# Optimization experiments

Measured on AMD Instinct MI355X. Metric: run time of the kernel, lower is better.

The kernel has to match this reference:

```python
import jax, jax.numpy as jnp
import numpy as np

N, E, F_IN, H, C = 10000, 640000, 128, 128, 40


def setup_inputs() -> dict:
    key = jax.random.key(0)
    ks = jax.random.split(key, 8)
    x = jax.random.normal(ks[0], (N, F_IN), dtype=jnp.float32)
    edge_index = jax.random.randint(ks[1], (2, E), 0, N, dtype=jnp.int64)
    W1 = jax.random.normal(ks[2], (F_IN, H), dtype=jnp.float32) / np.sqrt(F_IN)
    b1 = jnp.zeros((H,), dtype=jnp.float32)
    W2 = jax.random.normal(ks[3], (H, H), dtype=jnp.float32) / np.sqrt(H)
    b2 = jnp.zeros((H,), dtype=jnp.float32)
    Wc = jax.random.normal(ks[4], (H, C), dtype=jnp.float32) / np.sqrt(H)
    bc = jnp.zeros((C,), dtype=jnp.float32)
    return {"x": x, "edge_index": edge_index, "W1": W1, "b1": b1,
            "W2": W2, "b2": b2, "Wc": Wc, "bc": bc}


def _gcn_conv(x, src, dst, norm, W, b):
    # GCNConv: out = D^{-1/2}(A+I)D^{-1/2} (x @ W) + b
    h = x @ W                               # [N, H]
    msg = h[src] * norm[:, None]            # gather + per-edge normalize
    out = jax.ops.segment_sum(msg, dst, num_segments=N)  # scatter-add
    return out + b


def reference(x, edge_index, W1, b1, W2, b2, Wc, bc):
    # add self-loops (as PyG GCNConv does by default)
    loops = jnp.arange(N, dtype=edge_index.dtype)
    src = jnp.concatenate([edge_index[0], loops])   # [E+N]
    dst = jnp.concatenate([edge_index[1], loops])   # [E+N]
    # symmetric normalization deg^{-1/2} with self-loops included
    deg = jax.ops.segment_sum(jnp.ones_like(dst, dtype=x.dtype), dst, num_segments=N)
    dinv = jax.lax.rsqrt(deg)                       # deg >= 1 due to self-loops
    norm = dinv[src] * dinv[dst]                    # [E+N]

    h = _gcn_conv(x, src, dst, norm, W1, b1)
    h = jax.nn.relu(h)
    h = _gcn_conv(h, src, dst, norm, W2, b2)
    logits = h @ Wc + bc                            # [N, C]
    return jax.nn.log_softmax(logits, axis=1)
```

## Files before the change

### kernel.cpp

```cpp
#include <hip/hip_runtime.h>
#include <hip/hip_fp16.h>
#include <math.h>

#define FDIM 128
#define CDIM 40
#define DMAX 192
#define NMAX 10240
#define SLICE_SHIFT 14
#define SLICE_SZ (1 << SLICE_SHIFT)

__device__ __forceinline__ uint2 pack_half4(float4 v) {
    __half2 p0 = __float22half2_rn(make_float2(v.x, v.y));
    __half2 p1 = __float22half2_rn(make_float2(v.z, v.w));
    uint2 u;
    u.x = *(unsigned int*)&p0;
    u.y = *(unsigned int*)&p1;
    return u;
}

__device__ __forceinline__ void unpack_add4(float acc[8], uint4 r) {
    __half2* p = (__half2*)&r;
    #pragma unroll
    for (int q = 0; q < 4; ++q) {
        float2 f = __half22float2(p[q]);
        acc[2 * q]     += f.x;
        acc[2 * q + 1] += f.y;
    }
}

__global__ __launch_bounds__(256) void k_hist(
        const int* __restrict__ dst, unsigned short* __restrict__ lrank,
        int* __restrict__ cnt, int e, int n) {
    __shared__ int h[NMAX];
    int tid = threadIdx.x;
    for (int i = tid; i < n; i += 256) h[i] = 0;
    __syncthreads();
    int base = (int)blockIdx.x << SLICE_SHIFT;
    int end = base + SLICE_SZ; if (end > e) end = e;
    for (int i = base + tid * 4; i < end; i += 1024) {
        if (i + 3 < end) {
            int4 d = *(const int4*)(dst + i);
            int p0 = atomicAdd(&h[d.x], 1);
            int p1 = atomicAdd(&h[d.y], 1);
            int p2 = atomicAdd(&h[d.z], 1);
            int p3 = atomicAdd(&h[d.w], 1);
            ushort4 r;
            r.x = (unsigned short)p0; r.y = (unsigned short)p1;
            r.z = (unsigned short)p2; r.w = (unsigned short)p3;
            *(ushort4*)(lrank + i) = r;
        } else {
            for (int k = i; k < end; ++k)
                lrank[k] = (unsigned short)atomicAdd(&h[dst[k]], 1);
        }
    }
    __syncthreads();
    int* c = cnt + (size_t)blockIdx.x * n;
    for (int i = tid; i < n; i += 256) c[i] = h[i];
}

__global__ __launch_bounds__(256) void k_scan(
        int* __restrict__ cnt, int* __restrict__ deg, int nslice, int n) {
    int v = blockIdx.x * 256 + threadIdx.x;
    if (v >= n) return;
    int s = 0;
    for (int b = 0; b < nslice; ++b) {
        int t = cnt[(size_t)b * n + v];
        cnt[(size_t)b * n + v] = s;
        s += t;
    }
    deg[v] = s;
}

__global__ __launch_bounds__(256) void k_mega(
        const float* __restrict__ A, const float* __restrict__ W,
        const int* __restrict__ deg, uint2* __restrict__ h16, int n,
        const int* __restrict__ src, const int* __restrict__ dst,
        const unsigned short* __restrict__ lrank, const int* __restrict__ base,
        unsigned short* __restrict__ col, int e, int gemm_blocks) {
    __shared__ float As[32][FDIM];
    int tid = threadIdx.x;
    if ((int)blockIdx.x < gemm_blocks) {
        int r0 = blockIdx.x * 32;
        for (int t = tid; t < 32 * 32; t += 256) {
            int r = t >> 5, c4 = t & 31;
            int gr = r0 + r;
            float4 v = make_float4(0.f, 0.f, 0.f, 0.f);
            if (gr < n) v = ((const float4*)A)[(size_t)gr * 32 + c4];
            ((float4*)As[r])[c4] = v;
        }
        __syncthreads();
        int cb = (tid & 31) * 4;
        int rb = (tid >> 5) * 4;
        float4 acc0 = make_float4(0,0,0,0), acc1 = acc0, acc2 = acc0, acc3 = acc0;
        for (int k = 0; k < FDIM; ++k) {
            float4 w = *(const float4*)(W + k * FDIM + cb);
            float a0 = As[rb + 0][k], a1 = As[rb + 1][k];
            float a2 = As[rb + 2][k], a3 = As[rb + 3][k];
            acc0.x += a0 * w.x; acc0.y += a0 * w.y; acc0.z += a0 * w.z; acc0.w += a0 * w.w;
            acc1.x += a1 * w.x; acc1.y += a1 * w.y; acc1.z += a1 * w.z; acc1.w += a1 * w.w;
            acc2.x += a2 * w.x; acc2.y += a2 * w.y; acc2.z += a2 * w.z; acc2.w += a2 * w.w;
            acc3.x += a3 * w.x; acc3.y += a3 * w.y; acc3.z += a3 * w.z; acc3.w += a3 * w.w;
        }
        float4 accs[4] = {acc0, acc1, acc2, acc3};
        #pragma unroll
        for (int i = 0; i < 4; ++i) {
            int gr = r0 + rb + i;
            if (gr < n) {
                float dinv = rsqrtf((float)(deg[gr] + 1));
                float4 v = accs[i];
                v.x *= dinv; v.y *= dinv; v.z *= dinv; v.w *= dinv;
                h16[(size_t)gr * 32 + (cb >> 2)] = pack_half4(v);
            }
        }
    } else {
        int g = ((int)blockIdx.x - gemm_blocks) * 256 + tid;
        int i4 = g * 4;
        if (i4 + 3 < e) {
            const int* bs = base + (size_t)(i4 >> SLICE_SHIFT) * n;
            int4 d = ((const int4*)dst)[g];
            int4 s = ((const int4*)src)[g];
            ushort4 lr = ((const ushort4*)lrank)[g];
            int p0 = bs[d.x] + lr.x;
            int p1 = bs[d.y] + lr.y;
            int p2 = bs[d.z] + lr.z;
            int p3 = bs[d.w] + lr.w;
            if (p0 < DMAX) col[(size_t)d.x * DMAX + p0] = (unsigned short)s.x;
            if (p1 < DMAX) col[(size_t)d.y * DMAX + p1] = (unsigned short)s.y;
            if (p2 < DMAX) col[(size_t)d.z * DMAX + p2] = (unsigned short)s.z;
            if (p3 < DMAX) col[(size_t)d.w * DMAX + p3] = (unsigned short)s.w;
        } else if (i4 < e) {
            for (int k = i4; k < e; ++k) {
                int d = dst[k];
                int p = base[(size_t)(k >> SLICE_SHIFT) * n + d] + lrank[k];
                if (p < DMAX) col[(size_t)d * DMAX + p] = (unsigned short)src[k];
            }
        }
    }
}

template <bool RELU>
__device__ __forceinline__ void agg_gather(
        float out8[8], const uint4* __restrict__ hs,
        const unsigned short* __restrict__ col, const int* __restrict__ deg,
        const float* __restrict__ bias, int node, int l) {
    int dn = deg[node];
    float dinv = rsqrtf((float)(dn + 1));
    if (dn > DMAX) dn = DMAX;
    const uint4* cl8 = (const uint4*)(col + (size_t)node * DMAX);
    float a0[8], a1[8];
    #pragma unroll
    for (int q = 0; q < 8; ++q) { a0[q] = 0.f; a1[q] = 0.f; }
    unpack_add4(a0, hs[(size_t)node * 16 + l]);
    int j = 0;
    for (; j + 8 <= dn; j += 8) {
        uint4 c = cl8[j >> 3];
        int s0 = c.x & 0xFFFF, s1 = c.x >> 16;
        int s2 = c.y & 0xFFFF, s3 = c.y >> 16;
        int s4 = c.z & 0xFFFF, s5 = c.z >> 16;
        int s6 = c.w & 0xFFFF, s7 = c.w >> 16;
        uint4 q0 = hs[(size_t)s0 * 16 + l];
        uint4 q1 = hs[(size_t)s1 * 16 + l];
        uint4 q2 = hs[(size_t)s2 * 16 + l];
        uint4 q3 = hs[(size_t)s3 * 16 + l];
        uint4 q4 = hs[(size_t)s4 * 16 + l];
        uint4 q5 = hs[(size_t)s5 * 16 + l];
        uint4 q6 = hs[(size_t)s6 * 16 + l];
        uint4 q7 = hs[(size_t)s7 * 16 + l];
        unpack_add4(a0, q0); unpack_add4(a1, q1);
        unpack_add4(a0, q2); unpack_add4(a1, q3);
        unpack_add4(a0, q4); unpack_add4(a1, q5);
        unpack_add4(a0, q6); unpack_add4(a1, q7);
    }
    const unsigned short* cl = col + (size_t)node * DMAX;
    for (; j < dn; ++j) unpack_add4(a0, hs[(size_t)cl[j] * 16 + l]);
    float4 b0 = ((const float4*)bias)[2 * l];
    float4 b1 = ((const float4*)bias)[2 * l + 1];
    float bb[8] = {b0.x, b0.y, b0.z, b0.w, b1.x, b1.y, b1.z, b1.w};
    #pragma unroll
    for (int q = 0; q < 8; ++q) {
        float v = dinv * (a0[q] + a1[q]) + bb[q];
        out8[q] = RELU ? fmaxf(v, 0.f) : v;
    }
}

__global__ __launch_bounds__(128) void k_agg_gemm(
        const uint4* __restrict__ hs1, const unsigned short* __restrict__ col,
        const int* __restrict__ deg, const float* __restrict__ b1,
        const float* __restrict__ W2, uint2* __restrict__ hs2, int n) {
    __shared__ float As[8][FDIM + 4];
    __shared__ float dl[8];
    int tid = threadIdx.x;
    int grp = tid >> 4, l = tid & 15;
    int node = blockIdx.x * 8 + grp;
    if (node < n) {
        float r8[8];
        agg_gather<true>(r8, hs1, col, deg, b1, node, l);
        float4* dst4 = (float4*)&As[grp][8 * l];
        dst4[0] = make_float4(r8[0], r8[1], r8[2], r8[3]);
        dst4[1] = make_float4(r8[4], r8[5], r8[6], r8[7]);
        if (l == 0) dl[grp] = rsqrtf((float)(deg[node] + 1));
    }
    __syncthreads();
    int cb = (tid & 31) * 4;
    int rb = (tid >> 5) * 2;
    float4 acc0 = make_float4(0,0,0,0), acc1 = acc0;
    for (int k = 0; k < FDIM; ++k) {
        float4 w = *(const float4*)(W2 + k * FDIM + cb);
        float x0 = As[rb][k], x1 = As[rb + 1][k];
        acc0.x += x0 * w.x; acc0.y += x0 * w.y; acc0.z += x0 * w.z; acc0.w += x0 * w.w;
        acc1.x += x1 * w.x; acc1.y += x1 * w.y; acc1.z += x1 * w.z; acc1.w += x1 * w.w;
    }
    int g0 = blockIdx.x * 8 + rb;
    if (g0 < n) {
        float s = dl[rb];
        float4 v = acc0;
        v.x *= s; v.y *= s; v.z *= s; v.w *= s;
        hs2[(size_t)g0 * 32 + (cb >> 2)] = pack_half4(v);
    }
    if (g0 + 1 < n) {
        float s = dl[rb + 1];
        float4 v = acc1;
        v.x *= s; v.y *= s; v.z *= s; v.w *= s;
        hs2[(size_t)(g0 + 1) * 32 + (cb >> 2)] = pack_half4(v);
    }
}

__global__ __launch_bounds__(128) void k_agg_cls(
        const uint4* __restrict__ hs2, const unsigned short* __restrict__ col,
        const int* __restrict__ deg, const float* __restrict__ b2,
        const float* __restrict__ Wc, const float* __restrict__ bc,
        float* __restrict__ out, int n) {
    __shared__ float As[8][FDIM + 4];
    int tid = threadIdx.x;
    int grp = tid >> 4, l = tid & 15;
    int node = blockIdx.x * 8 + grp;
    if (node < n) {
        float r8[8];
        agg_gather<false>(r8, hs2, col, deg, b2, node, l);
        float4* dst4 = (float4*)&As[grp][8 * l];
        dst4[0] = make_float4(r8[0], r8[1], r8[2], r8[3]);
        dst4[1] = make_float4(r8[4], r8[5], r8[6], r8[7]);
    }
    __syncthreads();
    int wv = tid >> 6, lane = tid & 63;
    #pragma unroll
    for (int ii = 0; ii < 4; ++ii) {
        int li = wv * 4 + ii;
        int nd = blockIdx.x * 8 + li;
        if (nd >= n) continue;
        const float* row = As[li];
        int c = (lane < CDIM) ? lane : (lane - 24);
        float acc = bc[c];
        for (int k = 0; k < FDIM; k += 4) {
            float a0 = row[k + 0], a1 = row[k + 1];
            float a2 = row[k + 2], a3 = row[k + 3];
            acc += a0 * Wc[(k + 0) * CDIM + c];
            acc += a1 * Wc[(k + 1) * CDIM + c];
            acc += a2 * Wc[(k + 2) * CDIM + c];
            acc += a3 * Wc[(k + 3) * CDIM + c];
        }
        float lv = (lane < CDIM) ? acc : -INFINITY;
        float m = lv;
        for (int off = 32; off > 0; off >>= 1) m = fmaxf(m, __shfl_down(m, off));
        m = __shfl(m, 0);
        float e = (lane < CDIM) ? expf(lv - m) : 0.0f;
        float s = e;
        for (int off = 32; off > 0; off >>= 1) s += __shfl_down(s, off);
        s = __shfl(s, 0);
        if (lane < CDIM) out[(size_t)nd * CDIM + lane] = lv - m - logf(s);
    }
}


extern "C" void kernel_launch(void* const* d_in, const int* in_sizes, int n_in,
                              void* d_out, int out_size, void* d_ws, size_t ws_size,
                              hipStream_t stream) {
    const float* x  = (const float*)d_in[0];
    const int*   ei = (const int*)d_in[1];
    const float* W1 = (const float*)d_in[2];
    const float* b1 = (const float*)d_in[3];
    const float* W2 = (const float*)d_in[4];
    const float* b2 = (const float*)d_in[5];
    const float* Wc = (const float*)d_in[6];
    const float* bc = (const float*)d_in[7];
    float* out = (float*)d_out;

    const int N = in_sizes[0] / FDIM;
    const int E = in_sizes[1] / 2;
    const int* srcp = ei;
    const int* dstp = ei + E;
    const int NSLICE = (E + SLICE_SZ - 1) >> SLICE_SHIFT;

    char* ws = (char*)d_ws;
    auto alloc = [&](size_t bytes) {
        char* p = ws;
        ws += (bytes + 255) & ~(size_t)255;
        return p;
    };
    int*            deg   = (int*)           alloc((size_t)N * 4);
    int*            cnt   = (int*)           alloc((size_t)NSLICE * N * 4);
    unsigned short* lrank = (unsigned short*)alloc((size_t)E * 2);
    unsigned short* col   = (unsigned short*)alloc((size_t)N * DMAX * 2);
    uint4*          h1h   = (uint4*)         alloc((size_t)N * 256);
    uint4*          h2h   = (uint4*)         alloc((size_t)N * 256);

    k_hist<<<NSLICE, 256, 0, stream>>>(dstp, lrank, cnt, E, N);

    k_scan<<<(N + 255) / 256, 256, 0, stream>>>(cnt, deg, NSLICE, N);

    int gb = (N + 31) / 32;
    int fb = (E / 4 + 255) / 256;
    k_mega<<<gb + fb, 256, 0, stream>>>(
        x, W1, deg, (uint2*)h1h, N, srcp, dstp, lrank, cnt, col, E, gb);

    k_agg_gemm<<<(N + 7) / 8, 128, 0, stream>>>(
        h1h, col, deg, b1, W2, (uint2*)h2h, N);

    k_agg_cls<<<(N + 7) / 8, 128, 0, stream>>>(
        h2h, col, deg, b2, Wc, bc, out, N);
}
```

Measured before the change: 160.2 us.

## Split each node's neighbor gather across two thread groups in aggregation kernels

The aggregation kernels now use 256 threads per block with two 16-lane groups per node. Each group gathers alternate 8-neighbor chunks, and the two partial sums are combined in shared memory before the bias, ReLU and normalization are applied. The aim is to double the memory-level parallelism of the latency-bound random gathers, since average degree is about 64. The cost is an extra shared-memory pass and barrier, twice the shared memory per block, and a GEMM phase where each thread now produces one row instead of two.

```diff
diff --git a/kernel.cpp b/kernel.cpp
--- a/kernel.cpp
+++ b/kernel.cpp
@@ -138,114 +138,132 @@
     }
 }
 
-template <bool RELU>
-__device__ __forceinline__ void agg_gather(
-        float out8[8], const uint4* __restrict__ hs,
-        const unsigned short* __restrict__ col, const int* __restrict__ deg,
-        const float* __restrict__ bias, int node, int l) {
-    int dn = deg[node];
-    float dinv = rsqrtf((float)(dn + 1));
-    if (dn > DMAX) dn = DMAX;
-    const uint4* cl8 = (const uint4*)(col + (size_t)node * DMAX);
+__device__ __forceinline__ void agg_gather_half(
+        float a[8], const uint4* __restrict__ hs,
+        const unsigned short* __restrict__ col, int node, int l, int dn,
+        int half) {
     float a0[8], a1[8];
     #pragma unroll
     for (int q = 0; q < 8; ++q) { a0[q] = 0.f; a1[q] = 0.f; }
-    unpack_add4(a0, hs[(size_t)node * 16 + l]);
-    int j = 0;
-    for (; j + 8 <= dn; j += 8) {
-        uint4 c = cl8[j >> 3];
-        int s0 = c.x & 0xFFFF, s1 = c.x >> 16;
-        int s2 = c.y & 0xFFFF, s3 = c.y >> 16;
-        int s4 = c.z & 0xFFFF, s5 = c.z >> 16;
-        int s6 = c.w & 0xFFFF, s7 = c.w >> 16;
-        uint4 q0 = hs[(size_t)s0 * 16 + l];
-        uint4 q1 = hs[(size_t)s1 * 16 + l];
-        uint4 q2 = hs[(size_t)s2 * 16 + l];
-        uint4 q3 = hs[(size_t)s3 * 16 + l];
-        uint4 q4 = hs[(size_t)s4 * 16 + l];
-        uint4 q5 = hs[(size_t)s5 * 16 + l];
-        uint4 q6 = hs[(size_t)s6 * 16 + l];
-        uint4 q7 = hs[(size_t)s7 * 16 + l];
-        unpack_add4(a0, q0); unpack_add4(a1, q1);
-        unpack_add4(a0, q2); unpack_add4(a1, q3);
-        unpack_add4(a0, q4); unpack_add4(a1, q5);
-        unpack_add4(a0, q6); unpack_add4(a1, q7);
-    }
-    const unsigned short* cl = col + (size_t)node * DMAX;
-    for (; j < dn; ++j) unpack_add4(a0, hs[(size_t)cl[j] * 16 + l]);
-    float4 b0 = ((const float4*)bias)[2 * l];
-    float4 b1 = ((const float4*)bias)[2 * l + 1];
-    float bb[8] = {b0.x, b0.y, b0.z, b0.w, b1.x, b1.y, b1.z, b1.w};
+    if (half == 0) unpack_add4(a0, hs[(size_t)node * 16 + l]);
+    if (dn > DMAX) dn = DMAX;
+    const uint4* cl8 = (const uint4*)(col + (size_t)node * DMAX);
+    int nchunk = (dn + 7) >> 3;
+    for (int c = half; c < nchunk; c += 2) {
+        uint4 cc = cl8[c];
+        int cnt = dn - (c << 3);
+        if (cnt >= 8) {
+            int s0 = cc.x & 0xFFFF, s1 = cc.x >> 16;
+            int s2 = cc.y & 0xFFFF, s3 = cc.y >> 16;
+            int s4 = cc.z & 0xFFFF, s5 = cc.z >> 16;
+            int s6 = cc.w & 0xFFFF, s7 = cc.w >> 16;
+            uint4 q0 = hs[(size_t)s0 * 16 + l];
+            uint4 q1 = hs[(size_t)s1 * 16 + l];
+            uint4 q2 = hs[(size_t)s2 * 16 + l];
+            uint4 q3 = hs[(size_t)s3 * 16 + l];
+            uint4 q4 = hs[(size_t)s4 * 16 + l];
+            uint4 q5 = hs[(size_t)s5 * 16 + l];
+            uint4 q6 = hs[(size_t)s6 * 16 + l];
+            uint4 q7 = hs[(size_t)s7 * 16 + l];
+            unpack_add4(a0, q0); unpack_add4(a1, q1);
+            unpack_add4(a0, q2); unpack_add4(a1, q3);
+            unpack_add4(a0, q4); unpack_add4(a1, q5);
+            unpack_add4(a0, q6); unpack_add4(a1, q7);
+        } else {
+            union { uint4 v; unsigned short u[8]; } uu;
+            uu.v = cc;
+            for (int t = 0; t < cnt; ++t)
+                unpack_add4(a0, hs[(size_t)uu.u[t] * 16 + l]);
+        }
+    }
     #pragma unroll
-    for (int q = 0; q < 8; ++q) {
-        float v = dinv * (a0[q] + a1[q]) + bb[q];
-        out8[q] = RELU ? fmaxf(v, 0.f) : v;
-    }
-}
-
-__global__ __launch_bounds__(128) void k_agg_gemm(
+    for (int q = 0; q < 8; ++q) a[q] = a0[q] + a1[q];
+}
+
+__global__ __launch_bounds__(256) void k_agg_gemm(
         const uint4* __restrict__ hs1, const unsigned short* __restrict__ col,
         const int* __restrict__ deg, const float* __restrict__ b1,
         const float* __restrict__ W2, uint2* __restrict__ hs2, int n) {
-    __shared__ float As[8][FDIM + 4];
-    __shared__ float dl[8];
+    __shared__ float As[16][FDIM + 4];
     int tid = threadIdx.x;
-    int grp = tid >> 4, l = tid & 15;
-    int node = blockIdx.x * 8 + grp;
+    int slot = tid >> 4, l = tid & 15;
+    int node = blockIdx.x * 8 + (slot & 7);
+    int half = slot >> 3;
     if (node < n) {
-        float r8[8];
-        agg_gather<true>(r8, hs1, col, deg, b1, node, l);
-        float4* dst4 = (float4*)&As[grp][8 * l];
-        dst4[0] = make_float4(r8[0], r8[1], r8[2], r8[3]);
-        dst4[1] = make_float4(r8[4], r8[5], r8[6], r8[7]);
-        if (l == 0) dl[grp] = rsqrtf((float)(deg[node] + 1));
-    }
-    __syncthreads();
-    int cb = (tid & 31) * 4;
-    int rb = (tid >> 5) * 2;
-    float4 acc0 = make_float4(0,0,0,0), acc1 = acc0;
+        float a[8];
+        agg_gather_half(a, hs1, col, node, l, deg[node], half);
+        float4* d4 = (float4*)&As[slot][8 * l];
+        d4[0] = make_float4(a[0], a[1], a[2], a[3]);
+        d4[1] = make_float4(a[4], a[5], a[6], a[7]);
+    }
+    __syncthreads();
+    int r = tid >> 5;
+    int k0 = (tid & 31) * 4;
+    int g = blockIdx.x * 8 + r;
+    if (g < n) {
+        float di = rsqrtf((float)(deg[g] + 1));
+        float4 p0 = *(float4*)&As[r][k0];
+        float4 p1 = *(float4*)&As[r + 8][k0];
+        float4 b = *(const float4*)(b1 + k0);
+        float4 v;
+        v.x = fmaxf(di * (p0.x + p1.x) + b.x, 0.f);
+        v.y = fmaxf(di * (p0.y + p1.y) + b.y, 0.f);
+        v.z = fmaxf(di * (p0.z + p1.z) + b.z, 0.f);
+        v.w = fmaxf(di * (p0.w + p1.w) + b.w, 0.f);
+        *(float4*)&As[r][k0] = v;
+    }
+    __syncthreads();
+    float4 acc = make_float4(0, 0, 0, 0);
     for (int k = 0; k < FDIM; ++k) {
-        float4 w = *(const float4*)(W2 + k * FDIM + cb);
-        float x0 = As[rb][k], x1 = As[rb + 1][k];
-        acc0.x += x0 * w.x; acc0.y += x0 * w.y; acc0.z += x0 * w.z; acc0.w += x0 * w.w;
-        acc1.x += x1 * w.x; acc1.y += x1 * w.y; acc1.z += x1 * w.z; acc1.w += x1 * w.w;
-    }
-    int g0 = blockIdx.x * 8 + rb;
-    if (g0 < n) {
-        float s = dl[rb];
-        float4 v = acc0;
-        v.x *= s; v.y *= s; v.z *= s; v.w *= s;
-        hs2[(size_t)g0 * 32 + (cb >> 2)] = pack_half4(v);
-    }
-    if (g0 + 1 < n) {
-        float s = dl[rb + 1];
-        float4 v = acc1;
-        v.x *= s; v.y *= s; v.z *= s; v.w *= s;
-        hs2[(size_t)(g0 + 1) * 32 + (cb >> 2)] = pack_half4(v);
-    }
-}
-
-__global__ __launch_bounds__(128) void k_agg_cls(
+        float4 w = *(const float4*)(W2 + k * FDIM + k0);
+        float a = As[r][k];
+        acc.x += a * w.x; acc.y += a * w.y; acc.z += a * w.z; acc.w += a * w.w;
+    }
+    if (g < n) {
+        float di = rsqrtf((float)(deg[g] + 1));
+        acc.x *= di; acc.y *= di; acc.z *= di; acc.w *= di;
+        hs2[(size_t)g * 32 + (k0 >> 2)] = pack_half4(acc);
+    }
+}
+
+__global__ __launch_bounds__(256) void k_agg_cls(
         const uint4* __restrict__ hs2, const unsigned short* __restrict__ col,
         const int* __restrict__ deg, const float* __restrict__ b2,
         const float* __restrict__ Wc, const float* __restrict__ bc,
         float* __restrict__ out, int n) {
-    __shared__ float As[8][FDIM + 4];
+    __shared__ float As[16][FDIM + 4];
     int tid = threadIdx.x;
-    int grp = tid >> 4, l = tid & 15;
-    int node = blockIdx.x * 8 + grp;
+    int slot = tid >> 4, l = tid & 15;
+    int node = blockIdx.x * 8 + (slot & 7);
+    int half = slot >> 3;
     if (node < n) {
-        float r8[8];
-        agg_gather<false>(r8, hs2, col, deg, b2, node, l);
-        float4* dst4 = (float4*)&As[grp][8 * l];
-        dst4[0] = make_float4(r8[0], r8[1], r8[2], r8[3]);
-        dst4[1] = make_float4(r8[4], r8[5], r8[6], r8[7]);
+        float a[8];
+        agg_gather_half(a, hs2, col, node, l, deg[node], half);
+        float4* d4 = (float4*)&As[slot][8 * l];
+        d4[0] = make_float4(a[0], a[1], a[2], a[3]);
+        d4[1] = make_float4(a[4], a[5], a[6], a[7]);
+    }
+    __syncthreads();
+    int r = tid >> 5;
+    int k0 = (tid & 31) * 4;
+    int g = blockIdx.x * 8 + r;
+    if (g < n) {
+        float di = rsqrtf((float)(deg[g] + 1));
+        float4 p0 = *(float4*)&As[r][k0];
+        float4 p1 = *(float4*)&As[r + 8][k0];
+        float4 b = *(const float4*)(b2 + k0);
+        float4 v;
+        v.x = di * (p0.x + p1.x) + b.x;
+        v.y = di * (p0.y + p1.y) + b.y;
+        v.z = di * (p0.z + p1.z) + b.z;
+        v.w = di * (p0.w + p1.w) + b.w;
+        *(float4*)&As[r][k0] = v;
     }
     __syncthreads();
     int wv = tid >> 6, lane = tid & 63;
     #pragma unroll
-    for (int ii = 0; ii < 4; ++ii) {
-        int li = wv * 4 + ii;
+    for (int ii = 0; ii < 2; ++ii) {
+        int li = wv * 2 + ii;
         int nd = blockIdx.x * 8 + li;
         if (nd >= n) continue;
         const float* row = As[li];
@@ -313,9 +331,9 @@
     k_mega<<<gb + fb, 256, 0, stream>>>(
         x, W1, deg, (uint2*)h1h, N, srcp, dstp, lrank, cnt, col, E, gb);
 
-    k_agg_gemm<<<(N + 7) / 8, 128, 0, stream>>>(
+    k_agg_gemm<<<(N + 7) / 8, 256, 0, stream>>>(
         h1h, col, deg, b1, W2, (uint2*)h2h, N);
 
-    k_agg_cls<<<(N + 7) / 8, 128, 0, stream>>>(
+    k_agg_cls<<<(N + 7) / 8, 256, 0, stream>>>(
         h2h, col, deg, b2, Wc, bc, out, N);
 }
```

Result: slower. 212.2 us (+32.5%).
